# Optimization experiments

Measured on AMD Instinct MI355X. Metric: run time of the kernel, lower is better.

## Reference

```python
import jax, jax.numpy as jnp
import numpy as np

B, S, D_IN, D_OUT = 4, 2048, 1024, 1024
USE_MASK = True


def setup_inputs() -> dict:
    key = jax.random.key(0)
    ks = jax.random.split(key, 6)
    return {
        "inputs_for_keys": jax.random.normal(ks[0], (B, S, D_IN), jnp.float32),
        "inputs_for_values": jax.random.normal(ks[1], (B, S, D_IN), jnp.float32),
        "inputs_for_queries": jax.random.normal(ks[2], (B, S, D_IN), jnp.float32),
        "WK": jax.random.normal(ks[3], (D_IN, D_OUT), jnp.float32) * 0.1,
        "WV": jax.random.normal(ks[4], (D_IN, D_OUT), jnp.float32) * 0.1,
        "WQ": jax.random.normal(ks[5], (D_IN, D_OUT), jnp.float32) * 0.1,
    }


def reference(inputs_for_keys, inputs_for_values, inputs_for_queries, WK, WV, WQ):
    # projections: [B,S,Din] @ [Din,Dout] -> [B,S,Dout]
    K = jnp.einsum("bsd,de->bse", inputs_for_keys, WK)
    V = jnp.einsum("bsd,de->bse", inputs_for_values, WV)
    Q = jnp.einsum("bsd,de->bse", inputs_for_queries, WQ)

    dk = jnp.asarray(K.shape[2], jnp.float32)
    # scores: [B, Sq, Sk]
    score = jnp.einsum("bqd,bkd->bqk", Q, K) / jnp.sqrt(dk)
    if USE_MASK:
        # causal: -inf strictly above diagonal (j > i), matching the
        # transposed tril(-1) * -inf construction in the original.
        q_idx = jnp.arange(S)[:, None]
        k_idx = jnp.arange(S)[None, :]
        mask = jnp.where(k_idx > q_idx, -jnp.inf, 0.0).astype(score.dtype)
        score = score + mask[None, :, :]
    soft_score = jax.nn.softmax(score, axis=-1)
    return jnp.einsum("bqk,bkd->bqd", soft_score, V)
```

## Files before the change

### kernel.cpp

```cpp
#include <hip/hip_runtime.h>
#include <hip/hip_bf16.h>

typedef unsigned short u16;
typedef _Float16 f16;
typedef __attribute__((ext_vector_type(8))) short s16x8;
typedef __attribute__((ext_vector_type(8))) _Float16 f16x8;
typedef __attribute__((ext_vector_type(4))) float f32x4;
typedef __attribute__((ext_vector_type(4))) unsigned short u16x4;

template <typename T>
__device__ __forceinline__ auto mfma_try(T a, T b, f32x4 c, int)
    -> decltype(__builtin_amdgcn_mfma_f32_16x16x32_f16(a, b, c, 0, 0, 0)) {
  return __builtin_amdgcn_mfma_f32_16x16x32_f16(a, b, c, 0, 0, 0);
}
template <typename T>
__device__ __forceinline__ f32x4 mfma_try(T a, T b, f32x4 c, long) {
  return __builtin_amdgcn_mfma_f32_16x16x32_f16(
      __builtin_bit_cast(f16x8, a), __builtin_bit_cast(f16x8, b), c, 0, 0, 0);
}
__device__ __forceinline__ f32x4 MFMA16(s16x8 a, s16x8 b, f32x4 c) {
  return mfma_try(a, b, c, 0);
}

__device__ __forceinline__ void gload16(const void* g, void* s) {
  __builtin_amdgcn_global_load_lds(
      (const __attribute__((address_space(1))) void*)g,
      (__attribute__((address_space(3))) void*)s, 16, 0, 0);
}

__device__ __forceinline__ u16 f2h(float x) {
  f16 h = (f16)x;
  u16 u;
  __builtin_memcpy(&u, &h, 2);
  return u;
}
__device__ __forceinline__ float h2f(u16 u) {
  f16 h;
  __builtin_memcpy(&h, &u, 2);
  return (float)h;
}

#define LDS_SWZ(r, cb) ((cb) ^ (((r)&7) << 4))

struct Geom {
  int srow[4], scol[4];
  int w, l, wr, wc;
};

__device__ __forceinline__ Geom make_geom() {
  Geom g;
  int tid = threadIdx.x;
  g.w = tid >> 6; g.l = tid & 63;
  g.wr = g.w >> 1; g.wc = g.w & 1;
#pragma unroll
  for (int i = 0; i < 4; ++i) {
    int off = i * 4096 + g.w * 1024 + g.l * 16;
    int r = off >> 7, cb = off & 127;
    g.srow[i] = r;
    g.scol[i] = LDS_SWZ(r, cb) >> 1;
  }
  return g;
}

__device__ __forceinline__ void stage(const u16* pan, int ld, int k0,
                                      char* lds, const Geom& g) {
#pragma unroll
  for (int i = 0; i < 4; ++i)
    gload16(pan + (long)g.srow[i] * ld + k0 + g.scol[i],
            lds + i * 4096 + g.w * 1024);
}

__device__ __forceinline__ void compute_step(const char* lA, const char* lB,
                                             const Geom& g, f32x4 acc[4][4]) {
#pragma unroll
  for (int ks = 0; ks < 2; ++ks) {
    s16x8 af[4], bg[4];
#pragma unroll
    for (int m = 0; m < 4; ++m) {
      int r = g.wr * 64 + m * 16 + (g.l & 15);
      int cb = ks * 64 + ((g.l >> 4) << 4);
      af[m] = *(const s16x8*)(lA + r * 128 + LDS_SWZ(r, cb));
    }
#pragma unroll
    for (int n = 0; n < 4; ++n) {
      int r = g.wc * 64 + n * 16 + (g.l & 15);
      int cb = ks * 64 + ((g.l >> 4) << 4);
      bg[n] = *(const s16x8*)(lB + r * 128 + LDS_SWZ(r, cb));
    }
#pragma unroll
    for (int m = 0; m < 4; ++m)
#pragma unroll
      for (int n = 0; n < 4; ++n)
        acc[m][n] = MFMA16(af[m], bg[n], acc[m][n]);
  }
}

__device__ __forceinline__ void gemm_core(const u16* Apan, int lda,
                                          const u16* Bpan, int ldb, int nsteps,
                                          char* lA, char* lB, const Geom& g,
                                          f32x4 acc[4][4]) {
  stage(Apan, lda, 0, lA, g);
  stage(Bpan, ldb, 0, lB, g);
  __syncthreads();
  for (int t = 0; t < nsteps; ++t) {
    int cur = (t & 1) << 14;
    if (t + 1 < nsteps) {
      int nxt = ((t + 1) & 1) << 14;
      stage(Apan, lda, (t + 1) * 64, lA + nxt, g);
      stage(Bpan, ldb, (t + 1) * 64, lB + nxt, g);
    }
    compute_step(lA + cur, lB + cur, g, acc);
    if (t + 1 < nsteps) __syncthreads();
  }
}

__global__ __launch_bounds__(256, 2) void proj_kernel(
    const u16* __restrict__ xk, const u16* __restrict__ xq, const u16* __restrict__ xv,
    const u16* __restrict__ wk, const u16* __restrict__ wq, const u16* __restrict__ wv,
    u16* __restrict__ K, u16* __restrict__ Q, u16* __restrict__ Vt) {
  __shared__ char lds[65536];
  const int y = blockIdx.y;
  const u16* X = y == 0 ? xk : (y == 1 ? xq : xv);
  const u16* W = y == 0 ? wk : (y == 1 ? wq : wv);
  const int bx = blockIdx.x;
  const int swz = (bx & 7) * 64 + (bx >> 3);
  const int tm = swz >> 3, tn = swz & 7;
  Geom g = make_geom();
  f32x4 acc[4][4] = {};
  gemm_core(X + (long)tm * 128 * 1024, 1024, W + (long)tn * 128 * 1024, 1024,
            16, lds, lds + 32768, g, acc);
  const int rg0 = tm * 128 + g.wr * 64, cg0 = tn * 128 + g.wc * 64;
  if (y < 2) {
    u16* C = y == 0 ? K : Q;
#pragma unroll
    for (int m = 0; m < 4; ++m)
#pragma unroll
      for (int n = 0; n < 4; ++n)
#pragma unroll
        for (int j = 0; j < 4; ++j) {
          int rg = rg0 + m * 16 + ((g.l >> 4) << 2) + j;
          int cg = cg0 + n * 16 + (g.l & 15);
          C[(long)rg * 1024 + cg] = f2h(acc[m][n][j]);
        }
  } else {
#pragma unroll
    for (int m = 0; m < 4; ++m) {
      int rg = rg0 + m * 16 + ((g.l >> 4) << 2);
      int b = rg >> 11, rl = rg & 2047;
#pragma unroll
      for (int n = 0; n < 4; ++n) {
        int cg = cg0 + n * 16 + (g.l & 15);
        u16x4 pk;
#pragma unroll
        for (int j = 0; j < 4; ++j) pk[j] = f2h(acc[m][n][j]);
        *(u16x4*)(Vt + (long)b * (1024 * 2048) + (long)cg * 2048 + rl) = pk;
      }
    }
  }
}

__global__ __launch_bounds__(256, 2) void qkt_kernel(
    const u16* __restrict__ Q, const u16* __restrict__ K, u16* __restrict__ S) {
  __shared__ char lds[65536];
  const int bx = blockIdx.x;
  const int swz = (bx & 7) * 68 + (bx >> 3);
  const int b = swz / 136;
  int t = swz - b * 136;
  int tm = 0;
  while (t > tm) { t -= tm + 1; ++tm; }
  const int tn = t;
  Geom g = make_geom();
  f32x4 acc[4][4] = {};
  const u16* Qb = Q + (long)b * 2048 * 1024;
  const u16* Kb = K + (long)b * 2048 * 1024;
  gemm_core(Qb + (long)tm * 128 * 1024, 1024, Kb + (long)tn * 128 * 1024, 1024,
            16, lds, lds + 32768, g, acc);
  u16* Sb = S + (long)b * 2048 * 2048;
  const int rg0 = tm * 128 + g.wr * 64, cg0 = tn * 128 + g.wc * 64;
#pragma unroll
  for (int m = 0; m < 4; ++m)
#pragma unroll
    for (int n = 0; n < 4; ++n)
#pragma unroll
      for (int j = 0; j < 4; ++j) {
        int rg = rg0 + m * 16 + ((g.l >> 4) << 2) + j;
        int cg = cg0 + n * 16 + (g.l & 15);
        Sb[(long)rg * 2048 + cg] = f2h(acc[m][n][j]);
      }
}

__global__ __launch_bounds__(256, 2) void pv_kernel(
    const u16* __restrict__ P, const u16* __restrict__ Vt, float* __restrict__ O) {
  __shared__ char lds[65536];
  const int bx = blockIdx.x;
  const int swz = (bx & 7) * 64 + (bx >> 3);
  const int b = swz >> 7, loc = swz & 127;
  const int tm = loc >> 3, tn = loc & 7;
  Geom g = make_geom();
  f32x4 acc[4][4] = {};
  gemm_core(P + ((long)b * 2048 + tm * 128) * 2048, 2048,
            Vt + (long)b * 1024 * 2048 + (long)tn * 128 * 2048, 2048,
            (tm + 1) * 2, lds, lds + 32768, g, acc);
  const int rg0 = tm * 128 + g.wr * 64, cg0 = tn * 128 + g.wc * 64;
#pragma unroll
  for (int m = 0; m < 4; ++m)
#pragma unroll
    for (int n = 0; n < 4; ++n)
#pragma unroll
      for (int j = 0; j < 4; ++j) {
        int rg = rg0 + m * 16 + ((g.l >> 4) << 2) + j;
        int cg = cg0 + n * 16 + (g.l & 15);
        O[((long)b * 2048 + rg) * 1024 + cg] = acc[m][n][j];
      }
}

__global__ __launch_bounds__(256) void softmax_causal(
    const u16* __restrict__ S, u16* __restrict__ P) {
  const int row = blockIdx.x;
  const int i_q = row & 2047;
  const u16* sr = S + (long)row * 2048;
  u16* pr = P + (long)row * 2048;
  const int tid = threadIdx.x;
  const int l = tid & 63, w = tid >> 6;
  const int base = tid * 8;

  float v[8];
  float m = -INFINITY;
  if (base <= i_q) {
    s16x8 raw = *(const s16x8*)(sr + base);
#pragma unroll
    for (int j = 0; j < 8; ++j) {
      float x = h2f((u16)raw[j]);
      x = (base + j <= i_q) ? x : -INFINITY;
      v[j] = x;
      m = fmaxf(m, x);
    }
  } else {
#pragma unroll
    for (int j = 0; j < 8; ++j) v[j] = -INFINITY;
  }
  __shared__ float red[8];
  for (int o = 32; o; o >>= 1) m = fmaxf(m, __shfl_xor(m, o, 64));
  if (l == 0) red[w] = m;
  __syncthreads();
  m = fmaxf(fmaxf(red[0], red[1]), fmaxf(red[2], red[3]));

  float s = 0.f;
#pragma unroll
  for (int j = 0; j < 8; ++j) {
    v[j] = expf(v[j] - m);
    s += v[j];
  }
  for (int o = 32; o; o >>= 1) s += __shfl_xor(s, o, 64);
  if (l == 0) red[4 + w] = s;
  __syncthreads();
  s = (red[4] + red[5]) + (red[6] + red[7]);
  float inv = 1.0f / s;

  s16x8 o;
#pragma unroll
  for (int j = 0; j < 8; ++j) o[j] = (short)f2h(v[j] * inv);
  *(s16x8*)(pr + base) = o;
}

__global__ __launch_bounds__(256) void cast_all_kernel(
    const float* __restrict__ x0, const float* __restrict__ x1,
    const float* __restrict__ x2, u16* __restrict__ o0, u16* __restrict__ o1,
    u16* __restrict__ o2, const float* __restrict__ wk,
    const float* __restrict__ wv, const float* __restrict__ wq,
    u16* __restrict__ ok, u16* __restrict__ ov, u16* __restrict__ oq) {
  const int bid = blockIdx.x;
  if (bid < 12288) {
    const int y = bid >> 12;
    const float* in = y == 0 ? x0 : (y == 1 ? x1 : x2);
    u16* out = y == 0 ? o0 : (y == 1 ? o1 : o2);
    long i = ((long)(bid & 4095) * 256 + threadIdx.x) * 8;
    f32x4 a = *(const f32x4*)(in + i);
    f32x4 b = *(const f32x4*)(in + i + 4);
    s16x8 o;
#pragma unroll
    for (int j = 0; j < 4; ++j) {
      o[j] = (short)f2h(a[j]);
      o[4 + j] = (short)f2h(b[j]);
    }
    *(s16x8*)(out + i) = o;
  } else {
    __shared__ float tile[32][33];
    const int t = bid - 12288;
    const int z = t >> 10;
    const int loc = t & 1023;
    const int bx = loc & 31, by = loc >> 5;
    const float* w = z == 0 ? wk : (z == 1 ? wv : wq);
    u16* o = z == 0 ? ok : (z == 1 ? ov : oq);
    const float scale = (z == 2) ? 0.03125f : 1.0f;
    const int lx = threadIdx.x & 31, ly = threadIdx.x >> 5;
#pragma unroll
    for (int j = 0; j < 32; j += 8)
      tile[ly + j][lx] = w[(long)(by * 32 + ly + j) * 1024 + bx * 32 + lx];
    __syncthreads();
#pragma unroll
    for (int j = 0; j < 32; j += 8)
      o[(long)(bx * 32 + ly + j) * 1024 + by * 32 + lx] =
          f2h(tile[lx][ly + j] * scale);
  }
}

extern "C" void kernel_launch(void* const* d_in, const int* in_sizes, int n_in,
                              void* d_out, int out_size, void* d_ws, size_t ws_size,
                              hipStream_t stream) {
  const float* Xk = (const float*)d_in[0];
  const float* Xv = (const float*)d_in[1];
  const float* Xq = (const float*)d_in[2];
  const float* WK = (const float*)d_in[3];
  const float* WV = (const float*)d_in[4];
  const float* WQ = (const float*)d_in[5];

  const int Bn = 4, S = 2048, D = 1024;
  const long NX = (long)Bn * S * D;

  const size_t r0 = (size_t)Bn * S * S * 4;
  const size_t r1 = r0 + 3ull * D * D * 2;
  const size_t r2 = r1 + 2ull * NX * 2;
  const size_t NEED = r2 + (size_t)NX * 2;
  if (ws_size < NEED) {
    hipMemsetAsync(d_out, 0, (size_t)out_size * 4, stream);
    return;
  }
  char* ws = (char*)d_ws;
  u16* xkb = (u16*)ws;
  u16* xvb = xkb + NX;
  u16* xqb = xvb + NX;
  u16* scoresH = (u16*)ws;
  u16* wkt = (u16*)(ws + r0);
  u16* wvt = wkt + D * D;
  u16* wqt = wvt + D * D;
  u16* Kb = (u16*)(ws + r1);
  u16* Qb = Kb + NX;
  u16* Pb = (u16*)(ws + r1);
  u16* Vt = (u16*)(ws + r2);

  cast_all_kernel<<<dim3(15360), 256, 0, stream>>>(Xk, Xv, Xq, xkb, xvb, xqb,
                                                   WK, WV, WQ, wkt, wvt, wqt);
  proj_kernel<<<dim3(512, 3), 256, 0, stream>>>(xkb, xqb, xvb, wkt, wqt, wvt,
                                                Kb, Qb, Vt);
  qkt_kernel<<<dim3(544), 256, 0, stream>>>(Qb, Kb, scoresH);
  softmax_causal<<<dim3(8192), 256, 0, stream>>>(scoresH, Pb);
  pv_kernel<<<dim3(512), 256, 0, stream>>>(Pb, Vt, (float*)d_out);
}
```

Before: 163.2 us.

## Fuse softmax normalization into PV GEMM A-tile staging using row stats

```diff
diff --git a/kernel.cpp b/kernel.cpp
--- a/kernel.cpp
+++ b/kernel.cpp
@@ -43,7 +43,10 @@
 #define LDS_SWZ(r, cb) ((cb) ^ (((r)&7) << 4))
 
 struct Geom {
-  int srow[4], scol[4];
+  int srow[4];
+  int scol[4];
+  int scnat[4];
+  int wofs[4];
   int w, l, wr, wc;
 };
 
@@ -58,6 +61,8 @@
     int r = off >> 7, cb = off & 127;
     g.srow[i] = r;
     g.scol[i] = LDS_SWZ(r, cb) >> 1;
+    g.scnat[i] = cb >> 1;
+    g.wofs[i] = r * 128 + LDS_SWZ(r, cb);
   }
   return g;
 }
@@ -111,6 +116,56 @@
     }
     compute_step(lA + cur, lB + cur, g, acc);
     if (t + 1 < nsteps) __syncthreads();
+  }
+}
+
+__device__ __forceinline__ void a_issue16(const u16* pan, int k0, const Geom& g,
+                                          s16x8 (&ar)[4]) {
+#pragma unroll
+  for (int i = 0; i < 4; ++i)
+    ar[i] = *(const s16x8*)(pan + (long)g.srow[i] * 2048 + k0 + g.scnat[i]);
+}
+__device__ __forceinline__ void a_write_exp(char* lA, const Geom& g,
+                                            const s16x8 (&ar)[4], int k0,
+                                            const float (&m4)[4],
+                                            const float (&inv4)[4],
+                                            const int (&iq4)[4]) {
+#pragma unroll
+  for (int i = 0; i < 4; ++i) {
+    s16x8 h;
+#pragma unroll
+    for (int j = 0; j < 8; ++j) {
+      int k = k0 + g.scnat[i] + j;
+      float x = h2f((u16)ar[i][j]);
+      float p = __expf(x - m4[i]) * inv4[i];
+      p = (k <= iq4[i]) ? p : 0.0f;
+      h[j] = (short)f2h(p);
+    }
+    *(s16x8*)(lA + g.wofs[i]) = h;
+  }
+}
+
+__device__ __forceinline__ void gemm_core_pexp(
+    const u16* Ppan, const u16* Bpan, int ldb, int nsteps, char* lA, char* lB,
+    const Geom& g, f32x4 acc[4][4], const float (&m4)[4],
+    const float (&inv4)[4], const int (&iq4)[4]) {
+  s16x8 ar[4];
+  a_issue16(Ppan, 0, g, ar);
+  stage(Bpan, ldb, 0, lB, g);
+  a_write_exp(lA, g, ar, 0, m4, inv4, iq4);
+  __syncthreads();
+  for (int t = 0; t < nsteps; ++t) {
+    int cur = (t & 1) << 14;
+    int nxt = ((t + 1) & 1) << 14;
+    if (t + 1 < nsteps) {
+      a_issue16(Ppan, (t + 1) * 64, g, ar);
+      stage(Bpan, ldb, (t + 1) * 64, lB + nxt, g);
+    }
+    compute_step(lA + cur, lB + cur, g, acc);
+    if (t + 1 < nsteps) {
+      a_write_exp(lA + nxt, g, ar, (t + 1) * 64, m4, inv4, iq4);
+      __syncthreads();
+    }
   }
 }
 
@@ -190,17 +245,28 @@
 }
 
 __global__ __launch_bounds__(256, 2) void pv_kernel(
-    const u16* __restrict__ P, const u16* __restrict__ Vt, float* __restrict__ O) {
+    const u16* __restrict__ S, const u16* __restrict__ Vt,
+    const float* __restrict__ stats, float* __restrict__ O) {
   __shared__ char lds[65536];
   const int bx = blockIdx.x;
   const int swz = (bx & 7) * 64 + (bx >> 3);
   const int b = swz >> 7, loc = swz & 127;
   const int tm = loc >> 3, tn = loc & 7;
   Geom g = make_geom();
+  float m4[4], inv4[4];
+  int iq4[4];
+#pragma unroll
+  for (int i = 0; i < 4; ++i) {
+    int row = tm * 128 + g.srow[i];
+    iq4[i] = row;
+    const float* st = stats + ((long)b * 2048 + row) * 2;
+    m4[i] = st[0];
+    inv4[i] = st[1];
+  }
   f32x4 acc[4][4] = {};
-  gemm_core(P + ((long)b * 2048 + tm * 128) * 2048, 2048,
-            Vt + (long)b * 1024 * 2048 + (long)tn * 128 * 2048, 2048,
-            (tm + 1) * 2, lds, lds + 32768, g, acc);
+  gemm_core_pexp(S + ((long)b * 2048 + tm * 128) * 2048,
+                 Vt + (long)b * 1024 * 2048 + (long)tn * 128 * 2048, 2048,
+                 (tm + 1) * 2, lds, lds + 32768, g, acc, m4, inv4, iq4);
   const int rg0 = tm * 128 + g.wr * 64, cg0 = tn * 128 + g.wc * 64;
 #pragma unroll
   for (int m = 0; m < 4; ++m)
@@ -214,12 +280,11 @@
       }
 }
 
-__global__ __launch_bounds__(256) void softmax_causal(
-    const u16* __restrict__ S, u16* __restrict__ P) {
+__global__ __launch_bounds__(256) void rowstat_kernel(
+    const u16* __restrict__ S, float* __restrict__ stats) {
   const int row = blockIdx.x;
   const int i_q = row & 2047;
   const u16* sr = S + (long)row * 2048;
-  u16* pr = P + (long)row * 2048;
   const int tid = threadIdx.x;
   const int l = tid & 63, w = tid >> 6;
   const int base = tid * 8;
@@ -247,20 +312,15 @@
 
   float s = 0.f;
 #pragma unroll
-  for (int j = 0; j < 8; ++j) {
-    v[j] = expf(v[j] - m);
-    s += v[j];
-  }
+  for (int j = 0; j < 8; ++j) s += __expf(v[j] - m);
   for (int o = 32; o; o >>= 1) s += __shfl_xor(s, o, 64);
   if (l == 0) red[4 + w] = s;
   __syncthreads();
-  s = (red[4] + red[5]) + (red[6] + red[7]);
-  float inv = 1.0f / s;
-
-  s16x8 o;
-#pragma unroll
-  for (int j = 0; j < 8; ++j) o[j] = (short)f2h(v[j] * inv);
-  *(s16x8*)(pr + base) = o;
+  if (tid == 0) {
+    s = (red[4] + red[5]) + (red[6] + red[7]);
+    stats[(long)row * 2] = m;
+    stats[(long)row * 2 + 1] = 1.0f / s;
+  }
 }
 
 __global__ __launch_bounds__(256) void cast_all_kernel(
@@ -336,7 +396,7 @@
   u16* wqt = wvt + D * D;
   u16* Kb = (u16*)(ws + r1);
   u16* Qb = Kb + NX;
-  u16* Pb = (u16*)(ws + r1);
+  float* stats = (float*)(ws + r1);
   u16* Vt = (u16*)(ws + r2);
 
   cast_all_kernel<<<dim3(15360), 256, 0, stream>>>(Xk, Xv, Xq, xkb, xvb, xqb,
@@ -344,6 +404,6 @@
   proj_kernel<<<dim3(512, 3), 256, 0, stream>>>(xkb, xqb, xvb, wkt, wqt, wvt,
                                                 Kb, Qb, Vt);
   qkt_kernel<<<dim3(544), 256, 0, stream>>>(Qb, Kb, scoresH);
-  softmax_causal<<<dim3(8192), 256, 0, stream>>>(scoresH, Pb);
-  pv_kernel<<<dim3(512), 256, 0, stream>>>(Pb, Vt, (float*)d_out);
-}
+  rowstat_kernel<<<dim3(8192), 256, 0, stream>>>(scoresH, stats);
+  pv_kernel<<<dim3(512), 256, 0, stream>>>(scoresH, Vt, stats, (float*)d_out);
+}
```

New measurement: 187.3 us. 14.7% more time.
